# Kernel optimization log

Hardware: AMD Instinct MI355X
Metric: run time of the kernel (lower is better)

Reference implementation:

```python
import jax, jax.numpy as jnp
import numpy as np

N_HEADS = 16


def setup_inputs() -> dict:
    key = jax.random.key(0)
    ks = jax.random.split(key, 11)
    B, S, D = 8, 1024, 1024
    scale = 1.0 / np.sqrt(D)
    inp = {
        "batch": jax.random.normal(ks[0], (B, S, D), jnp.float32),
        "lengths": jax.random.randint(ks[1], (B,), 1, S + 1, jnp.int32),
        "wq": jax.random.normal(ks[2], (D, D), jnp.float32) * scale,
        "bq": jax.random.normal(ks[3], (D,), jnp.float32) * 0.02,
        "wk": jax.random.normal(ks[4], (D, D), jnp.float32) * scale,
        "bk": jax.random.normal(ks[5], (D,), jnp.float32) * 0.02,
        "wv": jax.random.normal(ks[6], (D, D), jnp.float32) * scale,
        "bv": jax.random.normal(ks[7], (D,), jnp.float32) * 0.02,
        "w0": jax.random.normal(ks[8], (D, D), jnp.float32) * scale,
        "b0": jax.random.normal(ks[9], (D,), jnp.float32) * 0.02,
    }
    return inp


def reference(batch, lengths, wq, bq, wk, bk, wv, bv, w0, b0):
    B, S, D = batch.shape
    H = N_HEADS
    dk = D // H
    q = (batch @ wq + bq).reshape(B, S, H, dk)
    k = (batch @ wk + bk).reshape(B, S, H, dk)
    v = (batch @ wv + bv).reshape(B, S, H, dk)
    # scores[b,h,s,q] = q_s . k_q  (no 1/sqrt(d_k) scaling, as in original)
    scores = jnp.einsum('bshd,bqhd->bhsq', q, k)
    rows = jnp.arange(S)[:, None]
    cols = jnp.arange(S)[None, :]
    causal = cols >= rows + 1                                   # [S,S]
    pad = jnp.arange(S)[None, :] >= lengths[:, None]            # [B,S] over key axis
    mask = causal[None, None, :, :] | pad[:, None, None, :]     # [B,1->H,S,S]
    scores = jnp.where(mask, -jnp.inf, scores)
    attn = jax.nn.softmax(scores, axis=-1)                      # [B,H,S,S]
    # Original uses einsum('bhss,bshd->bshd') -> diagonal of attention matrix
    attn_diag = jnp.diagonal(attn, axis1=2, axis2=3)            # [B,H,S]
    weighted = jnp.einsum('bhs,bshd->bshd', attn_diag, v)       # [B,S,H,dk]
    concated = weighted.reshape(B, S, D)
    return concated @ w0 + b0
```

## Files before the change

### kernel.cpp

```cpp
#include <hip/hip_runtime.h>
#include <hip/hip_bf16.h>
#include <stdint.h>
#include <math.h>

typedef short short8 __attribute__((ext_vector_type(8)));
typedef float f32x4 __attribute__((ext_vector_type(4)));
typedef unsigned short u16;

__device__ __forceinline__ u16 f2bf(float f) {
    unsigned u = __float_as_uint(f);
    unsigned r = 0x7FFFu + ((u >> 16) & 1u);
    return (u16)((u + r) >> 16);
}
__device__ __forceinline__ float bf2f(u16 h) {
    return __uint_as_float((unsigned)h << 16);
}

#define GL_LDS16(g, l)                                                         \
    __builtin_amdgcn_global_load_lds(                                          \
        (const __attribute__((address_space(1))) void*)(g),                    \
        (__attribute__((address_space(3))) void*)(l), 16, 0, 0)

__global__ __launch_bounds__(256) void k_prep(
    const float* __restrict__ batch, u16* __restrict__ Ab, int nconv,
    const float* __restrict__ wq, const float* __restrict__ wk,
    const float* __restrict__ wv, const float* __restrict__ w0,
    u16* __restrict__ wcat, u16* __restrict__ w0T, int Dim) {
    __shared__ float tile[64][65];
    const int bid = blockIdx.x;
    const int t = threadIdx.x;
    if (bid < nconv) {
        int i = bid * 256 + t;
        const float4* s = (const float4*)batch + (size_t)i * 2;
        float4 a = s[0], b = s[1];
        uint4 o;
        o.x = (unsigned)f2bf(a.x) | ((unsigned)f2bf(a.y) << 16);
        o.y = (unsigned)f2bf(a.z) | ((unsigned)f2bf(a.w) << 16);
        o.z = (unsigned)f2bf(b.x) | ((unsigned)f2bf(b.y) << 16);
        o.w = (unsigned)f2bf(b.z) | ((unsigned)f2bf(b.w) << 16);
        ((uint4*)Ab)[i] = o;
        return;
    }
    const int id = bid - nconv;
    const int w = id >> 8, r = id & 255;
    const float* W = (w == 0) ? wq : (w == 1) ? wk : (w == 2) ? wv : w0;
    u16* WT = (w == 3) ? w0T : wcat + (size_t)w * Dim * Dim;
    const int k0 = (r & 15) * 64, n0 = (r >> 4) * 64;
    const int col = t & 63, rb = t >> 6;
#pragma unroll
    for (int i = 0; i < 16; ++i) {
        int rr = i * 4 + rb;
        tile[rr][col] = W[(size_t)(k0 + rr) * Dim + n0 + col];
    }
    __syncthreads();
#pragma unroll
    for (int i = 0; i < 16; ++i) {
        int rr = i * 4 + rb;
        WT[(size_t)(n0 + rr) * Dim + k0 + col] = f2bf(tile[col][rr]);
    }
}

template <int FUSED>
__global__ __launch_bounds__(512) void k_gemm8(
    const u16* __restrict__ A, const u16* __restrict__ BT,
    const float* __restrict__ b1, const float* __restrict__ b2,
    const float* __restrict__ b3,
    u16* __restrict__ Qh, u16* __restrict__ Ql,
    u16* __restrict__ Kh, u16* __restrict__ Kl,
    u16* __restrict__ Vb, float* __restrict__ C,
    int K, int ldo) {
    __shared__ __align__(16) u16 ldsbuf[36864];

    const int wg = blockIdx.x;
    const int xcd = wg & 7, idc = wg >> 3;
    const int ml = idc & 3, nbn = idc >> 2;
    const int m0 = ((xcd << 2) + ml) << 8;
    const int n0 = nbn << 7;
    const int t = threadIdx.x;
    const int lane = t & 63, wave = t >> 6;
    const int wr = wave >> 1, wc = wave & 1;
    const int r16 = lane & 15, kq = lane >> 4;
    const int nt = K >> 6;
    const int np = nt << 1;

    int offA[4], offB[4];
#pragma unroll
    for (int mi = 0; mi < 4; ++mi) {
        int row = wr * 64 + mi * 16 + r16;
        offA[mi] = row * 32 + ((kq ^ ((row >> 1) & 3)) << 3);
    }
#pragma unroll
    for (int n = 0; n < 4; ++n) {
        int row = wc * 64 + n * 16 + r16;
        offB[n] = row * 32 + ((kq ^ ((row >> 1) & 3)) << 3);
    }

    f32x4 acc[4][4];
#pragma unroll
    for (int m = 0; m < 4; ++m)
#pragma unroll
        for (int n = 0; n < 4; ++n) acc[m][n] = (f32x4){0.f, 0.f, 0.f, 0.f};

    auto stage = [&](int h) {
        const int buf = h % 3;
        const int kt = ((h >> 1) << 6) + ((h & 1) << 5);
        u16* Abase = ldsbuf + buf * 12288;
        u16* Bbase = ldsbuf + buf * 12288 + 8192;
#pragma unroll
        for (int r = 0; r < 2; ++r) {
            int li = (r << 9) + t;
            int row = li >> 2;
            int kk = ((li & 3) ^ ((row >> 1) & 3)) << 3;
            GL_LDS16(A + (size_t)(m0 + row) * K + kt + kk,
                     Abase + ((li & ~63) << 3));
        }
        {
            int li = t;
            int row = li >> 2;
            int kk = ((li & 3) ^ ((row >> 1) & 3)) << 3;
            GL_LDS16(BT + (size_t)(n0 + row) * K + kt + kk,
                     Bbase + ((li & ~63) << 3));
        }
    };

    stage(0);
    stage(1);

    for (int p = 0; p < np; ++p) {
        if (p + 1 < np)
            asm volatile("s_waitcnt vmcnt(3)" ::: "memory");
        else
            asm volatile("s_waitcnt vmcnt(0)" ::: "memory");
        __builtin_amdgcn_sched_barrier(0);
        __builtin_amdgcn_s_barrier();
        __builtin_amdgcn_sched_barrier(0);

        const u16* base = ldsbuf + (p % 3) * 12288;
        short8 a[4], bfr[4];
#pragma unroll
        for (int mi = 0; mi < 4; ++mi)
            a[mi] = *(const short8*)(base + offA[mi]);
#pragma unroll
        for (int n = 0; n < 4; ++n)
            bfr[n] = *(const short8*)(base + 8192 + offB[n]);

        if (p + 2 < np) stage(p + 2);

        asm volatile("s_waitcnt lgkmcnt(0)" ::: "memory");
        __builtin_amdgcn_sched_barrier(0);
        __builtin_amdgcn_s_setprio(1);
#pragma unroll
        for (int mi = 0; mi < 4; ++mi)
#pragma unroll
            for (int n = 0; n < 4; ++n)
                acc[mi][n] = __builtin_amdgcn_mfma_f32_16x16x32_bf16(
                    a[mi], bfr[n], acc[mi][n], 0, 0, 0);
        __builtin_amdgcn_s_setprio(0);
        __builtin_amdgcn_sched_barrier(0);
    }

    if (FUSED) {
        const int seg = n0 >> 10;
        const float* bias = (seg == 0) ? b1 : (seg == 1) ? b2 : b3;
        u16* oh = (seg == 0) ? Qh : (seg == 1) ? Kh : Vb;
        u16* ol = (seg == 0) ? Ql : Kl;
        const int nc0 = n0 & 1023;
        const int nplanes = (seg < 2) ? 2 : 1;
        u16* lds = ldsbuf;
        for (int p = 0; p < nplanes; ++p) {
            __syncthreads();
#pragma unroll
            for (int n = 0; n < 4; ++n) {
                int col = wc * 64 + n * 16 + r16;
                float bvv = bias[nc0 + col];
#pragma unroll
                for (int mi = 0; mi < 4; ++mi) {
                    int row = wr * 64 + mi * 16 + kq * 4;
#pragma unroll
                    for (int j = 0; j < 4; ++j) {
                        float val = acc[mi][n][j] + bvv;
                        u16 hi = f2bf(val);
                        u16 w = p ? f2bf(val - bf2f(hi)) : hi;
                        lds[(row + j) * 128 + col] = w;
                    }
                }
            }
            __syncthreads();
            u16* dst = p ? ol : oh;
#pragma unroll
            for (int i = 0; i < 8; ++i) {
                int li = (i << 9) + t;
                int row = li >> 4, ch = li & 15;
                short8 v = *(const short8*)&lds[row * 128 + ch * 8];
                *(short8*)(dst + (size_t)(m0 + row) * ldo + nc0 + ch * 8) = v;
            }
        }
    } else {
#pragma unroll
        for (int n = 0; n < 4; ++n) {
            int col = n0 + wc * 64 + n * 16 + r16;
            float bvv = b1[col];
#pragma unroll
            for (int mi = 0; mi < 4; ++mi) {
                int row = m0 + wr * 64 + mi * 16 + kq * 4;
#pragma unroll
                for (int j = 0; j < 4; ++j)
                    C[(size_t)(row + j) * ldo + col] = acc[mi][n][j] + bvv;
            }
        }
    }
}

__global__ __launch_bounds__(256, 2) void k_scores(
    const u16* __restrict__ Qhi, const u16* __restrict__ Qlo,
    const u16* __restrict__ Khi, const u16* __restrict__ Klo,
    const u16* __restrict__ Vb, const int* __restrict__ lengths,
    u16* __restrict__ Wt, int S, int D) {
    __shared__ __align__(16) u16 KsHi[64 * 64];
    __shared__ __align__(16) u16 KsLo[64 * 64];
    __shared__ float dbuf[128];

    const int wg = blockIdx.x;
    const int xcd = wg & 7, idc = wg >> 3;
    const int bh = (xcd << 4) + (idc >> 3);
    const int bx = idc & 7;
    const int b = bh >> 4, h = bh & 15;
    const int nchunk = S >> 6;
    const int a0 = bx << 6;
    const int b0 = (nchunk - 1 - bx) << 6;

    const int t = threadIdx.x;
    const int lane = t & 63, wave = t >> 6;
    const int r16 = lane & 15, h2 = lane >> 4;
    const int len = lengths[b];

    short8 qh[2][2], ql[2][2];
#pragma unroll
    for (int m = 0; m < 2; ++m) {
        const int qm = m ? b0 : a0;
        const int row = qm + (wave << 4) + r16;
#pragma unroll
        for (int ks = 0; ks < 2; ++ks) {
            size_t off = ((size_t)(b * S) + row) * D + (h << 6) + (ks << 5) + (h2 << 3);
            qh[m][ks] = *(const short8*)(Qhi + off);
            ql[m][ks] = *(const short8*)(Qlo + off);
        }
    }

    float sum[2][4];
    float diag[2] = {-1e30f, -1e30f};
#pragma unroll
    for (int m = 0; m < 2; ++m)
#pragma unroll
        for (int r = 0; r < 4; ++r) sum[m][r] = 0.f;

    const int jmax = min(b0 + 63, len - 1);
    for (int j0 = 0; j0 <= jmax; j0 += 64) {
        __syncthreads();
#pragma unroll
        for (int p = 0; p < 2; ++p) {
            const int base_row = p * 32 + wave * 8;
            const int row = base_row + (lane >> 3);
            const int lc = (lane & 7) ^ (row & 7);
            size_t g = ((size_t)(b * S) + j0 + row) * D + (h << 6) + (lc << 3);
            GL_LDS16(Khi + g, &KsHi[base_row * 64]);
            GL_LDS16(Klo + g, &KsLo[base_row * 64]);
        }
        __syncthreads();

        f32x4 acc[2][4];
#pragma unroll
        for (int m = 0; m < 2; ++m)
#pragma unroll
            for (int n = 0; n < 4; ++n) acc[m][n] = (f32x4){0.f, 0.f, 0.f, 0.f};

#pragma unroll
        for (int ks = 0; ks < 2; ++ks) {
            short8 kh[4], kl[4];
#pragma unroll
            for (int n = 0; n < 4; ++n) {
                int row = (n << 4) + r16;
                int lc = (ks << 2) + h2;
                int phys = (row << 7) + ((lc ^ (row & 7)) << 4);
                kh[n] = *(const short8*)((const char*)KsHi + phys);
                kl[n] = *(const short8*)((const char*)KsLo + phys);
            }
#pragma unroll
            for (int m = 0; m < 2; ++m) {
                const int qm = m ? b0 : a0;
                if (j0 > qm) continue;
#pragma unroll
                for (int n = 0; n < 4; ++n) {
                    if (j0 + (n << 4) > qm + (wave << 4) + 15) continue;
                    acc[m][n] = __builtin_amdgcn_mfma_f32_16x16x32_bf16(qh[m][ks], kh[n], acc[m][n], 0, 0, 0);
                    acc[m][n] = __builtin_amdgcn_mfma_f32_16x16x32_bf16(qh[m][ks], kl[n], acc[m][n], 0, 0, 0);
                    acc[m][n] = __builtin_amdgcn_mfma_f32_16x16x32_bf16(ql[m][ks], kh[n], acc[m][n], 0, 0, 0);
                }
            }
        }

        const bool pad = (j0 + 64 > len);
#pragma unroll
        for (int m = 0; m < 2; ++m) {
            const int qm = m ? b0 : a0;
            if (j0 > qm) continue;
            const bool causal = (j0 == qm);
            if (causal || pad) {
#pragma unroll
                for (int n = 0; n < 4; ++n)
#pragma unroll
                    for (int r = 0; r < 4; ++r) {
                        int j = j0 + (n << 4) + r16;
                        int s = qm + (wave << 4) + (h2 << 2) + r;
                        if (j > s || j >= len) acc[m][n][r] = -1e30f;
                    }
                if (causal) {
#pragma unroll
                    for (int r = 0; r < 4; ++r)
                        if (r16 == (h2 << 2) + r) {
#pragma unroll
                            for (int n = 0; n < 4; ++n)
                                if (n == wave) diag[m] = acc[m][n][r];
                        }
                }
            }
#pragma unroll
            for (int r = 0; r < 4; ++r)
                sum[m][r] += __expf(acc[m][0][r]) + __expf(acc[m][1][r]) +
                             __expf(acc[m][2][r]) + __expf(acc[m][3][r]);
        }
    }

#pragma unroll
    for (int m = 0; m < 2; ++m)
#pragma unroll
        for (int r = 0; r < 4; ++r) {
            float sv = sum[m][r];
            sv += __shfl_xor(sv, 1);
            sv += __shfl_xor(sv, 2);
            sv += __shfl_xor(sv, 4);
            sv += __shfl_xor(sv, 8);
            sum[m][r] = sv;
        }

#pragma unroll
    for (int m = 0; m < 2; ++m)
#pragma unroll
        for (int r = 0; r < 4; ++r)
            if (r16 == (h2 << 2) + r)
                dbuf[(m << 6) + (wave << 4) + r16] = __expf(diag[m]) / sum[m][r];
    __syncthreads();

#pragma unroll
    for (int i = 0; i < 8; ++i) {
        int ri = i * 16 + (t >> 4);
        int c4 = (t & 15) << 2;
        int srow = (ri < 64) ? a0 + ri : b0 + ri - 64;
        float dv = dbuf[ri];
        const uint2 vv = *(const uint2*)(Vb + ((size_t)(b * S) + srow) * D + (h << 6) + c4);
        float x0 = bf2f((u16)(vv.x & 0xffffu)), x1 = bf2f((u16)(vv.x >> 16));
        float x2 = bf2f((u16)(vv.y & 0xffffu)), x3 = bf2f((u16)(vv.y >> 16));
        uint2 o;
        o.x = (unsigned)f2bf(x0 * dv) | ((unsigned)f2bf(x1 * dv) << 16);
        o.y = (unsigned)f2bf(x2 * dv) | ((unsigned)f2bf(x3 * dv) << 16);
        *(uint2*)(Wt + ((size_t)(b * S) + srow) * D + (h << 6) + c4) = o;
    }
}

extern "C" void kernel_launch(void* const* d_in, const int* in_sizes, int n_in,
                              void* d_out, int out_size, void* d_ws, size_t ws_size,
                              hipStream_t stream) {
    const float* batch = (const float*)d_in[0];
    const int* lengths = (const int*)d_in[1];
    const float* wq = (const float*)d_in[2];
    const float* bq = (const float*)d_in[3];
    const float* wk = (const float*)d_in[4];
    const float* bk = (const float*)d_in[5];
    const float* wv = (const float*)d_in[6];
    const float* bv = (const float*)d_in[7];
    const float* w0 = (const float*)d_in[8];
    const float* b0 = (const float*)d_in[9];

    const int D = in_sizes[3];
    const int B = in_sizes[1];
    const int S = in_sizes[0] / (B * D);
    const int H = 16;
    const int M = B * S;

    char* ws = (char*)d_ws;
    u16* Ab = (u16*)ws;    ws += (size_t)M * D * 2;
    u16* wcat = (u16*)ws;  ws += (size_t)3 * D * D * 2;
    u16* w0T = (u16*)ws;   ws += (size_t)D * D * 2;
    u16* Qhi = (u16*)ws;   ws += (size_t)M * D * 2;
    u16* Qlo = (u16*)ws;   ws += (size_t)M * D * 2;
    u16* Khi = (u16*)ws;   ws += (size_t)M * D * 2;
    u16* Klo = (u16*)ws;   ws += (size_t)M * D * 2;
    u16* Vb = (u16*)ws;    ws += (size_t)M * D * 2;
    u16* Wtb = (u16*)ws;   ws += (size_t)M * D * 2;

    const int nconv = M * D / 8 / 256;
    k_prep<<<nconv + 4 * (D / 64) * (D / 64), 256, 0, stream>>>(
        batch, Ab, nconv, wq, wk, wv, w0, wcat, w0T, D);

    k_gemm8<1><<<(M / 256) * (3 * D / 128), 512, 0, stream>>>(
        Ab, wcat, bq, bk, bv, Qhi, Qlo, Khi, Klo, Vb, nullptr, D, D);

    k_scores<<<(S / 128) * H * B, 256, 0, stream>>>(Qhi, Qlo, Khi, Klo, Vb,
                                                    lengths, Wtb, S, D);

    k_gemm8<0><<<(M / 256) * (D / 128), 512, 0, stream>>>(
        Wtb, w0T, b0, nullptr, nullptr, nullptr, nullptr, nullptr, nullptr, nullptr,
        (float*)d_out, D, D);
}
```

Measured before the change: 152.7 us.

## Use 256-thread GEMM blocks with larger per-wave tiles; double-buffer K tiles in scores

The GEMM kernel now runs with 4 waves per block instead of 8. Each wave computes 128x64 outputs with 8x4 MFMA accumulators, which raises register reuse of the B fragments and lets two blocks share a CU. The staging loops and vmcnt thresholds are adjusted to match. In the scores kernel the K hi/lo tiles are double-buffered, so the next tile's global-to-LDS load is issued before computing on the current one, overlapping memory with MFMA at the cost of twice the LDS and higher register pressure.

```diff
diff --git a/kernel.cpp b/kernel.cpp
--- a/kernel.cpp
+++ b/kernel.cpp
@@ -61,7 +61,7 @@
 }
 
 template <int FUSED>
-__global__ __launch_bounds__(512) void k_gemm8(
+__global__ __launch_bounds__(256, 2) void k_gemm8(
     const u16* __restrict__ A, const u16* __restrict__ BT,
     const float* __restrict__ b1, const float* __restrict__ b2,
     const float* __restrict__ b3,
@@ -83,10 +83,10 @@
     const int nt = K >> 6;
     const int np = nt << 1;
 
-    int offA[4], offB[4];
-#pragma unroll
-    for (int mi = 0; mi < 4; ++mi) {
-        int row = wr * 64 + mi * 16 + r16;
+    int offA[8], offB[4];
+#pragma unroll
+    for (int mi = 0; mi < 8; ++mi) {
+        int row = wr * 128 + mi * 16 + r16;
         offA[mi] = row * 32 + ((kq ^ ((row >> 1) & 3)) << 3);
     }
 #pragma unroll
@@ -95,9 +95,9 @@
         offB[n] = row * 32 + ((kq ^ ((row >> 1) & 3)) << 3);
     }
 
-    f32x4 acc[4][4];
-#pragma unroll
-    for (int m = 0; m < 4; ++m)
+    f32x4 acc[8][4];
+#pragma unroll
+    for (int m = 0; m < 8; ++m)
 #pragma unroll
         for (int n = 0; n < 4; ++n) acc[m][n] = (f32x4){0.f, 0.f, 0.f, 0.f};
 
@@ -105,17 +105,18 @@
         const int buf = h % 3;
         const int kt = ((h >> 1) << 6) + ((h & 1) << 5);
         u16* Abase = ldsbuf + buf * 12288;
-        u16* Bbase = ldsbuf + buf * 12288 + 8192;
-#pragma unroll
-        for (int r = 0; r < 2; ++r) {
-            int li = (r << 9) + t;
+        u16* Bbase = Abase + 8192;
+#pragma unroll
+        for (int r = 0; r < 4; ++r) {
+            int li = (r << 8) + t;
             int row = li >> 2;
             int kk = ((li & 3) ^ ((row >> 1) & 3)) << 3;
             GL_LDS16(A + (size_t)(m0 + row) * K + kt + kk,
                      Abase + ((li & ~63) << 3));
         }
-        {
-            int li = t;
+#pragma unroll
+        for (int r = 0; r < 2; ++r) {
+            int li = (r << 8) + t;
             int row = li >> 2;
             int kk = ((li & 3) ^ ((row >> 1) & 3)) << 3;
             GL_LDS16(BT + (size_t)(n0 + row) * K + kt + kk,
@@ -128,7 +129,7 @@
 
     for (int p = 0; p < np; ++p) {
         if (p + 1 < np)
-            asm volatile("s_waitcnt vmcnt(3)" ::: "memory");
+            asm volatile("s_waitcnt vmcnt(6)" ::: "memory");
         else
             asm volatile("s_waitcnt vmcnt(0)" ::: "memory");
         __builtin_amdgcn_sched_barrier(0);
@@ -136,9 +137,9 @@
         __builtin_amdgcn_sched_barrier(0);
 
         const u16* base = ldsbuf + (p % 3) * 12288;
-        short8 a[4], bfr[4];
-#pragma unroll
-        for (int mi = 0; mi < 4; ++mi)
+        short8 a[8], bfr[4];
+#pragma unroll
+        for (int mi = 0; mi < 8; ++mi)
             a[mi] = *(const short8*)(base + offA[mi]);
 #pragma unroll
         for (int n = 0; n < 4; ++n)
@@ -150,7 +151,7 @@
         __builtin_amdgcn_sched_barrier(0);
         __builtin_amdgcn_s_setprio(1);
 #pragma unroll
-        for (int mi = 0; mi < 4; ++mi)
+        for (int mi = 0; mi < 8; ++mi)
 #pragma unroll
             for (int n = 0; n < 4; ++n)
                 acc[mi][n] = __builtin_amdgcn_mfma_f32_16x16x32_bf16(
@@ -174,8 +175,8 @@
                 int col = wc * 64 + n * 16 + r16;
                 float bvv = bias[nc0 + col];
 #pragma unroll
-                for (int mi = 0; mi < 4; ++mi) {
-                    int row = wr * 64 + mi * 16 + kq * 4;
+                for (int mi = 0; mi < 8; ++mi) {
+                    int row = wr * 128 + mi * 16 + kq * 4;
 #pragma unroll
                     for (int j = 0; j < 4; ++j) {
                         float val = acc[mi][n][j] + bvv;
@@ -188,8 +189,8 @@
             __syncthreads();
             u16* dst = p ? ol : oh;
 #pragma unroll
-            for (int i = 0; i < 8; ++i) {
-                int li = (i << 9) + t;
+            for (int i = 0; i < 16; ++i) {
+                int li = (i << 8) + t;
                 int row = li >> 4, ch = li & 15;
                 short8 v = *(const short8*)&lds[row * 128 + ch * 8];
                 *(short8*)(dst + (size_t)(m0 + row) * ldo + nc0 + ch * 8) = v;
@@ -201,8 +202,8 @@
             int col = n0 + wc * 64 + n * 16 + r16;
             float bvv = b1[col];
 #pragma unroll
-            for (int mi = 0; mi < 4; ++mi) {
-                int row = m0 + wr * 64 + mi * 16 + kq * 4;
+            for (int mi = 0; mi < 8; ++mi) {
+                int row = m0 + wr * 128 + mi * 16 + kq * 4;
 #pragma unroll
                 for (int j = 0; j < 4; ++j)
                     C[(size_t)(row + j) * ldo + col] = acc[mi][n][j] + bvv;
@@ -216,8 +217,8 @@
     const u16* __restrict__ Khi, const u16* __restrict__ Klo,
     const u16* __restrict__ Vb, const int* __restrict__ lengths,
     u16* __restrict__ Wt, int S, int D) {
-    __shared__ __align__(16) u16 KsHi[64 * 64];
-    __shared__ __align__(16) u16 KsLo[64 * 64];
+    __shared__ __align__(16) u16 KsHi[2][4096];
+    __shared__ __align__(16) u16 KsLo[2][4096];
     __shared__ float dbuf[128];
 
     const int wg = blockIdx.x;
@@ -254,19 +255,27 @@
 #pragma unroll
         for (int r = 0; r < 4; ++r) sum[m][r] = 0.f;
 
-    const int jmax = min(b0 + 63, len - 1);
-    for (int j0 = 0; j0 <= jmax; j0 += 64) {
-        __syncthreads();
+    auto stage_k = [&](int j0, int bufi) {
 #pragma unroll
         for (int p = 0; p < 2; ++p) {
             const int base_row = p * 32 + wave * 8;
             const int row = base_row + (lane >> 3);
             const int lc = (lane & 7) ^ (row & 7);
             size_t g = ((size_t)(b * S) + j0 + row) * D + (h << 6) + (lc << 3);
-            GL_LDS16(Khi + g, &KsHi[base_row * 64]);
-            GL_LDS16(Klo + g, &KsLo[base_row * 64]);
-        }
-        __syncthreads();
+            GL_LDS16(Khi + g, &KsHi[bufi][base_row * 64]);
+            GL_LDS16(Klo + g, &KsLo[bufi][base_row * 64]);
+        }
+    };
+
+    const int jmax = min(b0 + 63, len - 1);
+    stage_k(0, 0);
+    for (int j0 = 0; j0 <= jmax; j0 += 64) {
+        const int tb = (j0 >> 6) & 1;
+        asm volatile("s_waitcnt vmcnt(0)" ::: "memory");
+        __builtin_amdgcn_sched_barrier(0);
+        __builtin_amdgcn_s_barrier();
+        __builtin_amdgcn_sched_barrier(0);
+        if (j0 + 64 <= jmax) stage_k(j0 + 64, tb ^ 1);
 
         f32x4 acc[2][4];
 #pragma unroll
@@ -282,8 +291,8 @@
                 int row = (n << 4) + r16;
                 int lc = (ks << 2) + h2;
                 int phys = (row << 7) + ((lc ^ (row & 7)) << 4);
-                kh[n] = *(const short8*)((const char*)KsHi + phys);
-                kl[n] = *(const short8*)((const char*)KsLo + phys);
+                kh[n] = *(const short8*)((const char*)&KsHi[tb][0] + phys);
+                kl[n] = *(const short8*)((const char*)&KsLo[tb][0] + phys);
             }
 #pragma unroll
             for (int m = 0; m < 2; ++m) {
@@ -402,13 +411,13 @@
     k_prep<<<nconv + 4 * (D / 64) * (D / 64), 256, 0, stream>>>(
         batch, Ab, nconv, wq, wk, wv, w0, wcat, w0T, D);
 
-    k_gemm8<1><<<(M / 256) * (3 * D / 128), 512, 0, stream>>>(
+    k_gemm8<1><<<(M / 256) * (3 * D / 128), 256, 0, stream>>>(
         Ab, wcat, bq, bk, bv, Qhi, Qlo, Khi, Klo, Vb, nullptr, D, D);
 
     k_scores<<<(S / 128) * H * B, 256, 0, stream>>>(Qhi, Qlo, Khi, Klo, Vb,
                                                     lengths, Wtb, S, D);
 
-    k_gemm8<0><<<(M / 256) * (D / 128), 512, 0, stream>>>(
+    k_gemm8<0><<<(M / 256) * (D / 128), 256, 0, stream>>>(
         Wtb, w0T, b0, nullptr, nullptr, nullptr, nullptr, nullptr, nullptr, nullptr,
         (float*)d_out, D, D);
 }
```

Measured after the change: 175.8 us. +15.1%, slower.
